# Kernel tuning notes

Measured on AMD Instinct MI355X. Metric: run time of the kernel, lower is better.

Reference implementation:

```python
import jax, jax.numpy as jnp
import numpy as np

B, T, C, H = 4, 2048, 1024, 16
D = C // H  # head_dim = 64
ROPE_BASE = 10000.0


def _rope_cos_sin(T, D, dtype):
    # inv_freq: (D/2,), freqs: (T, D/2) -> cos/sin tiled to (T, D)
    inv_freq = 1.0 / (ROPE_BASE ** (jnp.arange(0, D, 2, dtype=jnp.float32) / D))
    freqs = jnp.arange(T, dtype=jnp.float32)[:, None] * inv_freq[None, :]
    emb = jnp.concatenate([freqs, freqs], axis=-1)  # (T, D)
    return jnp.cos(emb).astype(dtype), jnp.sin(emb).astype(dtype)


def _rotate_half(x):
    x1, x2 = jnp.split(x, 2, axis=-1)
    return jnp.concatenate([-x2, x1], axis=-1)


def setup_inputs() -> dict:
    key = jax.random.key(0)
    k1, k2, k3 = jax.random.split(key, 3)
    x = jax.random.normal(k1, (B, T, C), dtype=jnp.float32)
    W_qkv = jax.random.normal(k2, (C, 3 * C), dtype=jnp.float32) * (C ** -0.5)
    b_qkv = jnp.zeros((3 * C,), dtype=jnp.float32)
    W_out = jax.random.normal(k3, (C, C), dtype=jnp.float32) * (C ** -0.5)
    b_out = jnp.zeros((C,), dtype=jnp.float32)
    return {"x": x, "W_qkv": W_qkv, "b_qkv": b_qkv, "W_out": W_out, "b_out": b_out}


def reference(x, W_qkv, b_qkv, W_out, b_out):
    Bx, Tx, Cx = x.shape
    qkv = x @ W_qkv + b_qkv                                   # (B, T, 3C)
    qkv = qkv.reshape(Bx, Tx, 3, H, D).transpose(2, 0, 3, 1, 4)  # (3, B, H, T, D)
    q, k, v = qkv[0], qkv[1], qkv[2]

    cos, sin = _rope_cos_sin(Tx, D, x.dtype)                  # (T, D) each
    q = q * cos + _rotate_half(q) * sin
    k = k * cos + _rotate_half(k) * sin

    # NOTE: original code has no 1/sqrt(D) scaling — faithful reproduction.
    att = jnp.einsum('bhtd,bhsd->bhts', q, k)                 # (B, H, T, T)
    causal = jnp.tril(jnp.ones((Tx, Tx), dtype=bool))
    att = jnp.where(causal[None, None, :, :], att, -jnp.inf)
    att = jax.nn.softmax(att, axis=-1)
    y = jnp.einsum('bhts,bhsd->bhtd', att, v)                 # (B, H, T, D)
    y = y.transpose(0, 2, 1, 3).reshape(Bx, Tx, Cx)
    return y @ W_out + b_out
```

## Files before the change

### kernel.cpp

```cpp
#include <hip/hip_runtime.h>
#include <math.h>

#define NB    4
#define T_SEQ 2048
#define CDIM  1024
#define NH    16
#define DH    64
#define NQKV  3072

typedef short bf16x8 __attribute__((ext_vector_type(8)));
typedef float f32x4  __attribute__((ext_vector_type(4)));

#define GLOBAL_AS __attribute__((address_space(1)))
#define LDS_AS    __attribute__((address_space(3)))

__device__ __forceinline__ void async16(const void* g, void* l) {
  __builtin_amdgcn_global_load_lds((const GLOBAL_AS void*)g, (LDS_AS void*)l, 16, 0, 0);
}

__device__ __forceinline__ unsigned short f2bf(float f) {
  unsigned u = __float_as_uint(f);
  unsigned r = u + 0x7FFF + ((u >> 16) & 1);
  return (unsigned short)(r >> 16);
}

#define SWZ8(row, c) ((((row) << 3) | ((c) ^ ((row) & 7))) << 3)

__global__ __launch_bounds__(256) void convert_bf16(
    const float* __restrict__ in, unsigned short* __restrict__ out, int n4) {
  int i = blockIdx.x * 256 + threadIdx.x;
  if (i >= n4) return;
  float4 v = ((const float4*)in)[i];
  ushort4 o;
  o.x = f2bf(v.x); o.y = f2bf(v.y); o.z = f2bf(v.z); o.w = f2bf(v.w);
  ((ushort4*)out)[i] = o;
}

__global__ __launch_bounds__(256) void transpose_to_bf16(
    const float* __restrict__ in, unsigned short* __restrict__ out, int K, int N) {
  __shared__ float tile[32][33];
  int n0 = blockIdx.x << 5, k0 = blockIdx.y << 5;
  int r  = threadIdx.x >> 3;
  int c4 = (threadIdx.x & 7) << 2;
  float4 v = *(const float4*)&in[(size_t)(k0 + r) * N + n0 + c4];
  tile[r][c4 + 0] = v.x; tile[r][c4 + 1] = v.y;
  tile[r][c4 + 2] = v.z; tile[r][c4 + 3] = v.w;
  __syncthreads();
  ushort4 o;
  o.x = f2bf(tile[c4 + 0][r]); o.y = f2bf(tile[c4 + 1][r]);
  o.z = f2bf(tile[c4 + 2][r]); o.w = f2bf(tile[c4 + 3][r]);
  *(ushort4*)&out[(size_t)(n0 + r) * K + k0 + c4] = o;
}

__global__ __launch_bounds__(256) void transpose_v(
    const unsigned short* __restrict__ v, unsigned short* __restrict__ vt) {
  __shared__ unsigned short tile[64][65];
  int bh = blockIdx.y;
  int t0 = blockIdx.x << 6;
  size_t ib = (size_t)bh * (T_SEQ * DH);
  int tid = threadIdx.x;
#pragma unroll
  for (int u = 0; u < 2; ++u) {
    int f = u * 256 + tid;
    int tr = f >> 3, c = f & 7;
    bf16x8 val = *(const bf16x8*)&v[ib + (size_t)(t0 + tr) * DH + c * 8];
#pragma unroll
    for (int j = 0; j < 8; ++j) tile[tr][c * 8 + j] = (unsigned short)val[j];
  }
  __syncthreads();
#pragma unroll
  for (int u = 0; u < 2; ++u) {
    int f = u * 256 + tid;
    int d = f >> 3, c = f & 7;
    bf16x8 o;
#pragma unroll
    for (int j = 0; j < 8; ++j) o[j] = (short)tile[c * 8 + j][d];
    *(bf16x8*)&vt[ib + (size_t)d * T_SEQ + t0 + c * 8] = o;
  }
}

#define GEMM_MAIN(Aptr, Btptr, KDIM)                                          \
  __shared__ short As[128 * 32];                                              \
  __shared__ short Bs[128 * 32];                                              \
  int m0 = blockIdx.y << 7, n0 = blockIdx.x << 7;                             \
  int tid = threadIdx.x;                                                      \
  int wave = tid >> 6, lane = tid & 63;                                       \
  int wm = wave & 1, wn = wave >> 1;                                          \
  int col = lane & 15, quad = lane >> 4;                                      \
  f32x4 acc[4][4];                                                            \
  _Pragma("unroll") for (int mt = 0; mt < 4; ++mt)                            \
  _Pragma("unroll") for (int nt = 0; nt < 4; ++nt)                            \
    acc[mt][nt] = (f32x4){0.f, 0.f, 0.f, 0.f};                                \
  for (int k0 = 0; k0 < KDIM; k0 += 32) {                                     \
    __syncthreads();                                                          \
    _Pragma("unroll") for (int u = 0; u < 2; ++u) {                           \
      int flat = u * 256 + wave * 64 + lane;                                  \
      int row = flat >> 2, ch = flat & 3;                                     \
      async16(&Aptr[(size_t)(m0 + row) * KDIM + k0 + ch * 8],                 \
              &As[(u * 256 + wave * 64) * 8]);                                \
      async16(&Btptr[(size_t)(n0 + row) * KDIM + k0 + ch * 8],                \
              &Bs[(u * 256 + wave * 64) * 8]);                                \
    }                                                                         \
    __syncthreads();                                                          \
    bf16x8 af[4], bfr[4];                                                     \
    _Pragma("unroll") for (int mt = 0; mt < 4; ++mt)                          \
      af[mt] = *(const bf16x8*)&As[(wm * 64 + mt * 16 + col) * 32 + quad * 8];\
    _Pragma("unroll") for (int nt = 0; nt < 4; ++nt)                          \
      bfr[nt] = *(const bf16x8*)&Bs[(wn * 64 + nt * 16 + col) * 32 + quad * 8];\
    _Pragma("unroll") for (int mt = 0; mt < 4; ++mt)                          \
      _Pragma("unroll") for (int nt = 0; nt < 4; ++nt)                        \
        acc[mt][nt] = __builtin_amdgcn_mfma_f32_16x16x32_bf16(                \
            af[mt], bfr[nt], acc[mt][nt], 0, 0, 0);                           \
  }

__global__ __launch_bounds__(256) void gemm_qkv_mfma(
    const unsigned short* __restrict__ A, const unsigned short* __restrict__ Bt,
    const float* __restrict__ bias,
    unsigned short* __restrict__ qb, unsigned short* __restrict__ kb,
    unsigned short* __restrict__ vb) {
  GEMM_MAIN(A, Bt, CDIM)
  int nn = n0 + wn * 64;
  int which = nn >> 10;
  int h = (nn >> 6) & 15;
  unsigned short* dst = (which == 0) ? qb : ((which == 1) ? kb : vb);
  float bv[4];
#pragma unroll
  for (int nt = 0; nt < 4; ++nt) bv[nt] = bias[nn + nt * 16 + col];
  if (which < 2) {
    float invf0 = expf((float)col * -0.28782313662425572f);
    float invf1 = expf((float)(col + 16) * -0.28782313662425572f);
#pragma unroll
    for (int mt = 0; mt < 4; ++mt) {
#pragma unroll
      for (int r = 0; r < 4; ++r) {
        int m = m0 + wm * 64 + mt * 16 + quad * 4 + r;
        int bidx = m >> 11, t = m & 2047;
        float x0 = acc[mt][0][r] + bv[0];
        float x1 = acc[mt][1][r] + bv[1];
        float x2 = acc[mt][2][r] + bv[2];
        float x3 = acc[mt][3][r] + bv[3];
        float s0a, c0a, s1a, c1a;
        sincosf((float)t * invf0, &s0a, &c0a);
        sincosf((float)t * invf1, &s1a, &c1a);
        size_t ro = (((size_t)bidx * NH + h) * T_SEQ + t) * DH;
        dst[ro + col]      = f2bf(x0 * c0a - x2 * s0a);
        dst[ro + col + 16] = f2bf(x1 * c1a - x3 * s1a);
        dst[ro + col + 32] = f2bf(x2 * c0a + x0 * s0a);
        dst[ro + col + 48] = f2bf(x3 * c1a + x1 * s1a);
      }
    }
  } else {
#pragma unroll
    for (int mt = 0; mt < 4; ++mt) {
#pragma unroll
      for (int r = 0; r < 4; ++r) {
        int m = m0 + wm * 64 + mt * 16 + quad * 4 + r;
        int bidx = m >> 11, t = m & 2047;
        size_t ro = (((size_t)bidx * NH + h) * T_SEQ + t) * DH;
        dst[ro + col]      = f2bf(acc[mt][0][r] + bv[0]);
        dst[ro + col + 16] = f2bf(acc[mt][1][r] + bv[1]);
        dst[ro + col + 32] = f2bf(acc[mt][2][r] + bv[2]);
        dst[ro + col + 48] = f2bf(acc[mt][3][r] + bv[3]);
      }
    }
  }
}

__global__ __launch_bounds__(256) void gemm_out_mfma(
    const unsigned short* __restrict__ A, const unsigned short* __restrict__ Bt,
    const float* __restrict__ bias, float* __restrict__ out) {
  GEMM_MAIN(A, Bt, CDIM)
#pragma unroll
  for (int nt = 0; nt < 4; ++nt) {
    int n = n0 + wn * 64 + nt * 16 + col;
    float bv = bias[n];
#pragma unroll
    for (int mt = 0; mt < 4; ++mt) {
#pragma unroll
      for (int r = 0; r < 4; ++r) {
        int m = m0 + wm * 64 + mt * 16 + quad * 4 + r;
        out[(size_t)m * CDIM + n] = acc[mt][nt][r] + bv;
      }
    }
  }
}

__global__ __launch_bounds__(256) void attn_mfma(
    const unsigned short* __restrict__ qg, const unsigned short* __restrict__ kg,
    const unsigned short* __restrict__ vtg, unsigned short* __restrict__ yb) {
  __shared__ short Qs[128 * 64];
  __shared__ short Ks[64 * 64];
  __shared__ short Vts[64 * 64];
  __shared__ short Ps[4][32][72];
  int tid = threadIdx.x;
  int wave = tid >> 6, lane = tid & 63;
  int col = lane & 15, quad = lane >> 4;
  int bh = blockIdx.x;
  int qblk = 15 - (int)blockIdx.y;
  int qb0 = qblk << 7;
  size_t base = (size_t)bh * (T_SEQ * DH);

#pragma unroll
  for (int u = 0; u < 4; ++u) {
    int ff = u * 256 + wave * 64 + lane;
    int row = ff >> 3, cl = ff & 7;
    int cg = cl ^ (row & 7);
    async16(&qg[base + (size_t)(qb0 + row) * DH + cg * 8],
            &Qs[(u * 256 + wave * 64) * 8]);
  }

  bf16x8 ones;
#pragma unroll
  for (int j = 0; j < 8; ++j) ones[j] = (short)0x3F80;

  f32x4 oc[2][4], lsum[2];
#pragma unroll
  for (int mf = 0; mf < 2; ++mf) {
    lsum[mf] = (f32x4){0.f, 0.f, 0.f, 0.f};
#pragma unroll
    for (int dt = 0; dt < 4; ++dt) oc[mf][dt] = (f32x4){0.f, 0.f, 0.f, 0.f};
  }

  int qlo = qb0 + wave * 32;
  int qhi = qlo + 31;
  int nkb = (qblk << 1) + 2;
  for (int kb = 0; kb < nkb; ++kb) {
    int s0 = kb << 6;
    __syncthreads();
#pragma unroll
    for (int u = 0; u < 2; ++u) {
      int ff = u * 256 + wave * 64 + lane;
      int row = ff >> 3, cl = ff & 7;
      int cg = cl ^ (row & 7);
      async16(&kg[base + (size_t)(s0 + row) * DH + cg * 8],
              &Ks[(u * 256 + wave * 64) * 8]);
      async16(&vtg[base + (size_t)row * T_SEQ + s0 + cg * 8],
              &Vts[(u * 256 + wave * 64) * 8]);
    }
    __syncthreads();
    if (s0 > qhi) continue;

    f32x4 sc[2][4];
#pragma unroll
    for (int mf = 0; mf < 2; ++mf)
#pragma unroll
      for (int nt = 0; nt < 4; ++nt) sc[mf][nt] = (f32x4){0.f, 0.f, 0.f, 0.f};
#pragma unroll
    for (int kc = 0; kc < 2; ++kc) {
      bf16x8 aq0 = *(const bf16x8*)&Qs[SWZ8(wave * 32 + col,      kc * 4 + quad)];
      bf16x8 aq1 = *(const bf16x8*)&Qs[SWZ8(wave * 32 + 16 + col, kc * 4 + quad)];
#pragma unroll
      for (int nt = 0; nt < 4; ++nt) {
        bf16x8 bk = *(const bf16x8*)&Ks[SWZ8(nt * 16 + col, kc * 4 + quad)];
        sc[0][nt] = __builtin_amdgcn_mfma_f32_16x16x32_bf16(aq0, bk, sc[0][nt], 0, 0, 0);
        sc[1][nt] = __builtin_amdgcn_mfma_f32_16x16x32_bf16(aq1, bk, sc[1][nt], 0, 0, 0);
      }
    }

    if (s0 + 63 > qlo) {
#pragma unroll
      for (int mf = 0; mf < 2; ++mf)
#pragma unroll
        for (int nt = 0; nt < 4; ++nt) {
          int s_glob = s0 + nt * 16 + col;
#pragma unroll
          for (int r = 0; r < 4; ++r)
            if (s_glob > qlo + mf * 16 + quad * 4 + r) sc[mf][nt][r] = -3.0e38f;
        }
    }

#pragma unroll
    for (int mf = 0; mf < 2; ++mf)
#pragma unroll
      for (int nt = 0; nt < 4; ++nt)
#pragma unroll
        for (int r = 0; r < 4; ++r)
          Ps[wave][mf * 16 + quad * 4 + r][nt * 16 + col] =
              (short)f2bf(__expf(sc[mf][nt][r]));

#pragma unroll
    for (int kc = 0; kc < 2; ++kc) {
      bf16x8 ap0 = *(const bf16x8*)&Ps[wave][col][kc * 32 + quad * 8];
      bf16x8 ap1 = *(const bf16x8*)&Ps[wave][16 + col][kc * 32 + quad * 8];
      lsum[0] = __builtin_amdgcn_mfma_f32_16x16x32_bf16(ap0, ones, lsum[0], 0, 0, 0);
      lsum[1] = __builtin_amdgcn_mfma_f32_16x16x32_bf16(ap1, ones, lsum[1], 0, 0, 0);
#pragma unroll
      for (int dt = 0; dt < 4; ++dt) {
        bf16x8 vb = *(const bf16x8*)&Vts[SWZ8(dt * 16 + col, kc * 4 + quad)];
        oc[0][dt] = __builtin_amdgcn_mfma_f32_16x16x32_bf16(ap0, vb, oc[0][dt], 0, 0, 0);
        oc[1][dt] = __builtin_amdgcn_mfma_f32_16x16x32_bf16(ap1, vb, oc[1][dt], 0, 0, 0);
      }
    }
  }

  int b = bh >> 4, h = bh & 15;
#pragma unroll
  for (int mf = 0; mf < 2; ++mf)
#pragma unroll
    for (int dt = 0; dt < 4; ++dt) {
      int d = dt * 16 + col;
#pragma unroll
      for (int r = 0; r < 4; ++r) {
        int t = qb0 + wave * 32 + mf * 16 + quad * 4 + r;
        yb[(((size_t)b * T_SEQ + t) * NH + h) * DH + d] =
            f2bf(oc[mf][dt][r] / lsum[mf][r]);
      }
    }
}

extern "C" void kernel_launch(void* const* d_in, const int* in_sizes, int n_in,
                              void* d_out, int out_size, void* d_ws, size_t ws_size,
                              hipStream_t stream) {
  const float* x     = (const float*)d_in[0];
  const float* W_qkv = (const float*)d_in[1];
  const float* b_qkv = (const float*)d_in[2];
  const float* W_out = (const float*)d_in[3];
  const float* b_out = (const float*)d_in[4];
  float* out = (float*)d_out;

  const size_t per = (size_t)NB * NH * T_SEQ * DH;
  unsigned short* xb  = (unsigned short*)d_ws;
  unsigned short* qb  = xb + per;
  unsigned short* kbf = qb + per;
  unsigned short* vbf = kbf + per;
  unsigned short* vtb = vbf + per;
  unsigned short* yb  = vtb + per;
  unsigned short* wqt = yb + per;
  unsigned short* wot = wqt + (size_t)NQKV * CDIM;

  convert_bf16<<<(int)(per / 4 / 256), 256, 0, stream>>>(x, xb, (int)(per / 4));
  transpose_to_bf16<<<dim3(NQKV / 32, CDIM / 32), 256, 0, stream>>>(W_qkv, wqt, CDIM, NQKV);
  transpose_to_bf16<<<dim3(CDIM / 32, CDIM / 32), 256, 0, stream>>>(W_out, wot, CDIM, CDIM);
  gemm_qkv_mfma<<<dim3(NQKV / 128, (NB * T_SEQ) / 128), 256, 0, stream>>>(
      xb, wqt, b_qkv, qb, kbf, vbf);
  transpose_v<<<dim3(T_SEQ / 64, NB * NH), 256, 0, stream>>>(vbf, vtb);
  attn_mfma<<<dim3(NB * NH, T_SEQ / 128), 256, 0, stream>>>(qb, kbf, vtb, yb);
  gemm_out_mfma<<<dim3(CDIM / 128, (NB * T_SEQ) / 128), 256, 0, stream>>>(
      yb, wot, b_out, out);
}
```

Before: 267.0 us.

## Double-buffer GEMM tiles with async LDS loads, swizzle, and larger 128x256 blocks

Replaces the single-buffered 128x128, K=32 GEMM mainloop with a double-buffered pipeline. The next K=64 tile is prefetched via global_load_lds while the current one is consumed, using manual vmcnt waits and barriers. The tile grows to 128x256 with 512 threads (8 waves), and LDS is XOR-swizzled to avoid bank conflicts. MFMA sections are raised in priority with s_setprio. This aims to hide global load latency and raise arithmetic intensity. The risks are more LDS per block (96KB), fewer blocks for the output GEMM (256 blocks), and fragile hand-written wait counts.

```diff
diff --git a/kernel.cpp b/kernel.cpp
--- a/kernel.cpp
+++ b/kernel.cpp
@@ -25,6 +25,9 @@
 }
 
 #define SWZ8(row, c) ((((row) << 3) | ((c) ^ ((row) & 7))) << 3)
+
+#define BARRIER()  asm volatile("s_barrier" ::: "memory")
+#define VMCNT(n)   asm volatile("s_waitcnt vmcnt(" #n ")" ::: "memory")
 
 __global__ __launch_bounds__(256) void convert_bf16(
     const float* __restrict__ in, unsigned short* __restrict__ out, int n4) {
@@ -79,46 +82,71 @@
   }
 }
 
-#define GEMM_MAIN(Aptr, Btptr, KDIM)                                          \
-  __shared__ short As[128 * 32];                                              \
-  __shared__ short Bs[128 * 32];                                              \
-  int m0 = blockIdx.y << 7, n0 = blockIdx.x << 7;                             \
+#define GEMM_PIPE(Aptr, Btptr)                                                \
+  __shared__ short As[2][128 * 64];                                           \
+  __shared__ short Bs[2][256 * 64];                                           \
+  int m0 = blockIdx.y << 7, n0 = blockIdx.x << 8;                             \
   int tid = threadIdx.x;                                                      \
   int wave = tid >> 6, lane = tid & 63;                                       \
-  int wm = wave & 1, wn = wave >> 1;                                          \
+  int wm = wave >> 2, wn = wave & 3;                                          \
   int col = lane & 15, quad = lane >> 4;                                      \
+  int srow = tid >> 3;                                                        \
+  int schunk = (tid & 7) ^ (srow & 7);                                        \
+  const unsigned short* aSrc = &Aptr[(size_t)(m0 + srow) * CDIM + schunk * 8];\
+  const unsigned short* bSrc = &Btptr[(size_t)(n0 + srow) * CDIM + schunk * 8];\
+  int d0 = wave * 512;  \
   f32x4 acc[4][4];                                                            \
   _Pragma("unroll") for (int mt = 0; mt < 4; ++mt)                            \
   _Pragma("unroll") for (int nt = 0; nt < 4; ++nt)                            \
     acc[mt][nt] = (f32x4){0.f, 0.f, 0.f, 0.f};                                \
-  for (int k0 = 0; k0 < KDIM; k0 += 32) {                                     \
-    __syncthreads();                                                          \
-    _Pragma("unroll") for (int u = 0; u < 2; ++u) {                           \
-      int flat = u * 256 + wave * 64 + lane;                                  \
-      int row = flat >> 2, ch = flat & 3;                                     \
-      async16(&Aptr[(size_t)(m0 + row) * KDIM + k0 + ch * 8],                 \
-              &As[(u * 256 + wave * 64) * 8]);                                \
-      async16(&Btptr[(size_t)(n0 + row) * KDIM + k0 + ch * 8],                \
-              &Bs[(u * 256 + wave * 64) * 8]);                                \
+    \
+  async16(aSrc,          &As[0][d0]);                                         \
+  async16(aSrc + 65536,  &As[0][d0 + 4096]);                                  \
+  async16(bSrc,          &Bs[0][d0]);                                         \
+  async16(bSrc + 65536,  &Bs[0][d0 + 4096]);                                  \
+  async16(bSrc + 131072, &Bs[0][d0 + 8192]);                                  \
+  async16(bSrc + 196608, &Bs[0][d0 + 12288]);                                 \
+  for (int kt = 0; kt < 16; ++kt) {                                           \
+    int p = kt & 1;                                                           \
+    if (kt < 15) {                                                            \
+      const unsigned short* a_ = aSrc + (kt + 1) * 64;                        \
+      const unsigned short* b_ = bSrc + (kt + 1) * 64;                        \
+      async16(a_,          &As[p ^ 1][d0]);                                   \
+      async16(a_ + 65536,  &As[p ^ 1][d0 + 4096]);                            \
+      async16(b_,          &Bs[p ^ 1][d0]);                                   \
+      async16(b_ + 65536,  &Bs[p ^ 1][d0 + 4096]);                            \
+      async16(b_ + 131072, &Bs[p ^ 1][d0 + 8192]);                            \
+      async16(b_ + 196608, &Bs[p ^ 1][d0 + 12288]);                           \
+      VMCNT(6);          \
+    } else {                                                                  \
+      VMCNT(0);                                         \
     }                                                                         \
-    __syncthreads();                                                          \
-    bf16x8 af[4], bfr[4];                                                     \
-    _Pragma("unroll") for (int mt = 0; mt < 4; ++mt)                          \
-      af[mt] = *(const bf16x8*)&As[(wm * 64 + mt * 16 + col) * 32 + quad * 8];\
-    _Pragma("unroll") for (int nt = 0; nt < 4; ++nt)                          \
-      bfr[nt] = *(const bf16x8*)&Bs[(wn * 64 + nt * 16 + col) * 32 + quad * 8];\
-    _Pragma("unroll") for (int mt = 0; mt < 4; ++mt)                          \
+    BARRIER();                           \
+    _Pragma("unroll") for (int ks = 0; ks < 2; ++ks) {                        \
+      bf16x8 af[4], bfr[4];                                                   \
+      _Pragma("unroll") for (int mt = 0; mt < 4; ++mt)                        \
+        af[mt] = *(const bf16x8*)&As[p][SWZ8(wm * 64 + mt * 16 + col,         \
+                                             ks * 4 + quad)];                 \
       _Pragma("unroll") for (int nt = 0; nt < 4; ++nt)                        \
-        acc[mt][nt] = __builtin_amdgcn_mfma_f32_16x16x32_bf16(                \
-            af[mt], bfr[nt], acc[mt][nt], 0, 0, 0);                           \
-  }
-
-__global__ __launch_bounds__(256) void gemm_qkv_mfma(
+        bfr[nt] = *(const bf16x8*)&Bs[p][SWZ8(wn * 64 + nt * 16 + col,        \
+                                              ks * 4 + quad)];                \
+      BARRIER();                                                              \
+      __builtin_amdgcn_s_setprio(1);                                          \
+      _Pragma("unroll") for (int mt = 0; mt < 4; ++mt)                        \
+        _Pragma("unroll") for (int nt = 0; nt < 4; ++nt)                      \
+          acc[mt][nt] = __builtin_amdgcn_mfma_f32_16x16x32_bf16(              \
+              af[mt], bfr[nt], acc[mt][nt], 0, 0, 0);                         \
+      __builtin_amdgcn_s_setprio(0);                                          \
+      BARRIER();                                                              \
+    }                                                                         \
+  }
+
+__global__ __launch_bounds__(512, 2) void gemm_qkv_mfma(
     const unsigned short* __restrict__ A, const unsigned short* __restrict__ Bt,
     const float* __restrict__ bias,
     unsigned short* __restrict__ qb, unsigned short* __restrict__ kb,
     unsigned short* __restrict__ vb) {
-  GEMM_MAIN(A, Bt, CDIM)
+  GEMM_PIPE(A, Bt)
   int nn = n0 + wn * 64;
   int which = nn >> 10;
   int h = (nn >> 6) & 15;
@@ -166,10 +194,10 @@
   }
 }
 
-__global__ __launch_bounds__(256) void gemm_out_mfma(
+__global__ __launch_bounds__(512, 2) void gemm_out_mfma(
     const unsigned short* __restrict__ A, const unsigned short* __restrict__ Bt,
     const float* __restrict__ bias, float* __restrict__ out) {
-  GEMM_MAIN(A, Bt, CDIM)
+  GEMM_PIPE(A, Bt)
 #pragma unroll
   for (int nt = 0; nt < 4; ++nt) {
     int n = n0 + wn * 64 + nt * 16 + col;
@@ -331,10 +359,10 @@
   convert_bf16<<<(int)(per / 4 / 256), 256, 0, stream>>>(x, xb, (int)(per / 4));
   transpose_to_bf16<<<dim3(NQKV / 32, CDIM / 32), 256, 0, stream>>>(W_qkv, wqt, CDIM, NQKV);
   transpose_to_bf16<<<dim3(CDIM / 32, CDIM / 32), 256, 0, stream>>>(W_out, wot, CDIM, CDIM);
-  gemm_qkv_mfma<<<dim3(NQKV / 128, (NB * T_SEQ) / 128), 256, 0, stream>>>(
+  gemm_qkv_mfma<<<dim3(NQKV / 256, (NB * T_SEQ) / 128), 512, 0, stream>>>(
       xb, wqt, b_qkv, qb, kbf, vbf);
   transpose_v<<<dim3(T_SEQ / 64, NB * NH), 256, 0, stream>>>(vbf, vtb);
   attn_mfma<<<dim3(NB * NH, T_SEQ / 128), 256, 0, stream>>>(qb, kbf, vtb, yb);
-  gemm_out_mfma<<<dim3(CDIM / 128, (NB * T_SEQ) / 128), 256, 0, stream>>>(
+  gemm_out_mfma<<<dim3(CDIM / 256, (NB * T_SEQ) / 128), 512, 0, stream>>>(
       yb, wot, b_out, out);
 }
```

New measurement: 286.8 us. 7.4% more time.
